# Optimization experiments

Measured on AMD Instinct MI355X. Metric: run time of the kernel, lower is better.

## Reference

```python
import jax, jax.numpy as jnp
import numpy as np

SEQ_LEN, BATCH, INPUT_SIZE, HIDDEN = 512, 64, 256, 512


def setup_inputs() -> dict:
    key = jax.random.key(0)
    ks = jax.random.split(key, 5)
    s_in = 1.0 / np.sqrt(INPUT_SIZE)
    s_h = 1.0 / np.sqrt(HIDDEN)
    x = jax.random.normal(ks[0], (SEQ_LEN, BATCH, INPUT_SIZE), dtype=jnp.float32)
    # gate order: f, i, o, c  (matches the torch module's lin_W*/lin_U*)
    Wx = jax.random.uniform(ks[1], (4, HIDDEN, INPUT_SIZE), jnp.float32, -s_in, s_in)
    bx = jax.random.uniform(ks[2], (4, HIDDEN), jnp.float32, -s_in, s_in)
    Wh = jax.random.uniform(ks[3], (4, HIDDEN, HIDDEN), jnp.float32, -s_h, s_h)
    bh = jax.random.uniform(ks[4], (4, HIDDEN), jnp.float32, -s_h, s_h)
    return {"x": x, "Wx": Wx, "bx": bx, "Wh": Wh, "bh": bh}


def reference(x, Wx, bx, Wh, bh):
    # x: [T, B, I]; Wx: [4, H, I]; Wh: [4, H, H]; biases: [4, H] (gate order f,i,o,c)
    T, B, _ = x.shape
    H = Wh.shape[-1]
    # Precompute input projections for all timesteps (batched GEMM): [T, 4, B, H]
    gx = jnp.einsum('tbi,ghi->tgbh', x, Wx) + bx[:, None, :]

    def step(carry, gx_t):
        h_prev, c_prev = carry
        gh = jnp.einsum('bh,gkh->gbk', h_prev, Wh) + bh[:, None, :]  # [4, B, H]
        g = gx_t + gh
        f = jax.nn.sigmoid(g[0])
        i = jax.nn.sigmoid(g[1])
        o = jax.nn.sigmoid(g[2])
        c = f * c_prev + i * jnp.tanh(g[3])
        h = o * jnp.tanh(c)
        return (h, c), h

    h0 = jnp.zeros((B, H), dtype=x.dtype)
    c0 = jnp.zeros((B, H), dtype=x.dtype)
    (h_last, c_last), h_seq = jax.lax.scan(step, (h0, c0), gx)
    return h_seq, h_last, c_last
```

## Files before the change

kernel.cpp:

```cpp
#include <hip/hip_runtime.h>
#include <hip/hip_cooperative_groups.h>
#include <math.h>

namespace cg = cooperative_groups;

#define TT 512
#define BB 64
#define II 256
#define HH 512

#define NTHREADS 512
#define NGRP 4
#define NCT  16
#define NBLOCKS (NGRP*NCT)

#define KPAD 776

typedef _Float16 f16x8 __attribute__((ext_vector_type(8)));
typedef _Float16 f16x4 __attribute__((ext_vector_type(4)));
typedef float    f32x4 __attribute__((ext_vector_type(4)));

__device__ __forceinline__ float sig_(float v)  { return 1.0f / (1.0f + __expf(-v)); }
__device__ __forceinline__ float tanh_(float v) { float e = __expf(2.0f * v); return 1.0f - 2.0f / (e + 1.0f); }

__global__ void __launch_bounds__(NTHREADS, 2)
lstm_mfma2(const float* __restrict__ x,
           const float* __restrict__ Wx,
           const float* __restrict__ bx,
           const float* __restrict__ Wh,
           const float* __restrict__ bh,
           float* __restrict__ out,
           unsigned int* __restrict__ flags,
           unsigned int* __restrict__ hbuf)
{
    __shared__ _Float16 AL[16 * KPAD];
    __shared__ float    exch[8 * 16 * 20];

    cg::grid_group grid = cg::this_grid();

    const int blk  = blockIdx.x;
    const int grp  = blk & 3;
    const int b0   = grp * 16;
    const int ct   = blk >> 2;
    const int hblk = ct * 32;

    const int tid = threadIdx.x;
    const int wv  = tid >> 6;
    const int L   = tid & 63;
    const int n   = L & 15;
    const int qd  = L >> 4;

    const int g  = n & 3;
    const int hu = hblk + wv * 4 + (n >> 2);
    f16x8 bfr[24];
    #pragma unroll
    for (int kc = 0; kc < 24; ++kc) {
        int k0 = kc * 32 + qd * 8;
        const float* src = (kc < 8)
            ? (Wx + ((size_t)g * HH + hu) * II + k0)
            : (Wh + ((size_t)g * HH + hu) * HH + (k0 - 256));
        float4 u0 = ((const float4*)src)[0];
        float4 u1 = ((const float4*)src)[1];
        f16x8 b = { (_Float16)u0.x, (_Float16)u0.y, (_Float16)u0.z, (_Float16)u0.w,
                    (_Float16)u1.x, (_Float16)u1.y, (_Float16)u1.z, (_Float16)u1.w };
        bfr[kc] = b;
    }

    const int be  = L >> 2;
    const int hle = L & 3;
    const int he  = hblk + wv * 4 + hle;
    float bias4[4];
    #pragma unroll
    for (int g2 = 0; g2 < 4; ++g2) bias4[g2] = bx[g2 * HH + he] + bh[g2 * HH + he];

    if (tid == 0)
        __hip_atomic_store(&flags[grp * 64 + ct], 0u,
                           __ATOMIC_RELAXED, __HIP_MEMORY_SCOPE_AGENT);
    grid.sync();

    const size_t HSEQ = (size_t)TT * BB * HH;
    float c_state = 0.0f;
    float* exchW = &exch[wv * 16 * 20];

    for (int t = 0; t < TT; ++t) {
        #pragma unroll
        for (int i = 0; i < 2; ++i) {
            int ch = tid + i * NTHREADS;
            int row = ch >> 6, pos = ch & 63;
            float4 v = ((const float4*)(x + ((size_t)t * BB + b0 + row) * II))[pos];
            f16x4 p = { (_Float16)v.x, (_Float16)v.y, (_Float16)v.z, (_Float16)v.w };
            *(f16x4*)&AL[row * KPAD + pos * 4] = p;
        }

        if (t > 0 && wv == 0) {
            const unsigned int* fp = flags + grp * 64;
            for (;;) {
                unsigned f = (L < NCT)
                    ? __hip_atomic_load(&fp[L], __ATOMIC_RELAXED, __HIP_MEMORY_SCOPE_AGENT)
                    : 0xFFFFFFFFu;
                if (__all((int)(f >= (unsigned)t))) break;
                __builtin_amdgcn_s_sleep(1);
            }
        }
        __syncthreads();

        if (t > 0) {
            const unsigned long long* hsrc =
                (const unsigned long long*)(hbuf + (size_t)(t & 1) * (BB * 256));
            #pragma unroll
            for (int i = 0; i < 4; ++i) {
                int ch = tid + i * NTHREADS;
                int row = ch >> 7, pos = ch & 127;
                unsigned long long u = __hip_atomic_load(
                    hsrc + (size_t)(b0 + row) * 128 + pos,
                    __ATOMIC_RELAXED, __HIP_MEMORY_SCOPE_AGENT);
                *(unsigned long long*)((char*)AL + row * (KPAD * 2) + II * 2 + pos * 8) = u;
            }
            __syncthreads();
        }

        const char* Ab = (const char*)AL + n * (KPAD * 2) + qd * 16;
        f32x4 acc = { 0.f, 0.f, 0.f, 0.f };
        #pragma unroll
        for (int kc = 0; kc < 8; ++kc) {
            f16x8 a = *(const f16x8*)(Ab + kc * 64);
            acc = __builtin_amdgcn_mfma_f32_16x16x32_f16(a, bfr[kc], acc, 0, 0, 0);
        }
        if (t > 0) {
            #pragma unroll
            for (int kc = 8; kc < 24; ++kc) {
                f16x8 a = *(const f16x8*)(Ab + kc * 64);
                acc = __builtin_amdgcn_mfma_f32_16x16x32_f16(a, bfr[kc], acc, 0, 0, 0);
            }
        }

        #pragma unroll
        for (int r = 0; r < 4; ++r)
            exchW[(qd * 4 + r) * 20 + n] = acc[r];
        float4 pre4 = *(const float4*)&exchW[be * 20 + hle * 4];

        float pf = pre4.x + bias4[0];
        float pi = pre4.y + bias4[1];
        float po = pre4.z + bias4[2];
        float pc = pre4.w + bias4[3];
        float fg = sig_(pf), ig = sig_(pi), og = sig_(po);
        float cn = fg * c_state + ig * tanh_(pc);
        float hv = og * tanh_(cn);
        c_state = cn;

        out[((size_t)t * BB + b0 + be) * HH + he] = hv;
        if (t == TT - 1) {
            size_t r = (size_t)(b0 + be) * HH + he;
            out[HSEQ + r] = hv;
            out[HSEQ + (size_t)BB * HH + r] = cn;
        }

        {
            union { _Float16 f; unsigned short u; } cv; cv.f = (_Float16)hv;
            unsigned mine  = cv.u;
            unsigned other = (unsigned)__shfl_xor((int)mine, 1, 64);
            if ((hle & 1) == 0) {
                unsigned pk = mine | (other << 16);
                unsigned int* hdst = hbuf + (size_t)((t + 1) & 1) * (BB * 256);
                __hip_atomic_store(&hdst[(unsigned)(b0 + be) * 256 + (unsigned)(he >> 1)],
                                   pk, __ATOMIC_RELAXED, __HIP_MEMORY_SCOPE_AGENT);
            }
        }

        __syncthreads();
        if (t != TT - 1 && tid == 0)
            __hip_atomic_store(&flags[grp * 64 + ct], (unsigned)(t + 1),
                               __ATOMIC_RELAXED, __HIP_MEMORY_SCOPE_AGENT);
    }
}

extern "C" void kernel_launch(void* const* d_in, const int* in_sizes, int n_in,
                              void* d_out, int out_size, void* d_ws, size_t ws_size,
                              hipStream_t stream)
{
    const float* x  = (const float*)d_in[0];
    const float* Wx = (const float*)d_in[1];
    const float* bx = (const float*)d_in[2];
    const float* Wh = (const float*)d_in[3];
    const float* bh = (const float*)d_in[4];
    float* out = (float*)d_out;

    unsigned int* flags = (unsigned int*)d_ws;
    unsigned int* hbuf  = (unsigned int*)((char*)d_ws + 4096);

    void* args[] = { (void*)&x, (void*)&Wx, (void*)&bx, (void*)&Wh, (void*)&bh,
                     (void*)&out, (void*)&flags, (void*)&hbuf };
    hipLaunchCooperativeKernel((const void*)lstm_mfma2,
                               dim3(NBLOCKS), dim3(NTHREADS),
                               args, 0, stream);
}
```

Baseline: 1.674 ms.

## Shorten LSTM step critical path: precompute x-projection before flag wait, load h directly into registers

Computes the input-projection MFMAs before spinning on the cross-block flags, so the x part overlaps with waiting on other blocks. The h operand is loaded straight from global memory into MFMA registers instead of being staged through LDS, which removes a barrier and an LDS round trip. Four independent accumulators break the MFMA dependency chain. Output stores move after the flag publish, and syncthreads is replaced by lighter custom barriers. The risks are more register pressure from holding the h fragments and subtle memory-ordering issues from the hand-written barriers.

Result: slower. 4.675 ms (+179.3%).

```diff
diff --git a/kernel.cpp b/kernel.cpp
--- a/kernel.cpp
+++ b/kernel.cpp
@@ -14,7 +14,7 @@
 #define NCT  16
 #define NBLOCKS (NGRP*NCT)
 
-#define KPAD 776
+#define XPAD 264
 
 typedef _Float16 f16x8 __attribute__((ext_vector_type(8)));
 typedef _Float16 f16x4 __attribute__((ext_vector_type(4)));
@@ -23,8 +23,22 @@
 __device__ __forceinline__ float sig_(float v)  { return 1.0f / (1.0f + __expf(-v)); }
 __device__ __forceinline__ float tanh_(float v) { float e = __expf(2.0f * v); return 1.0f - 2.0f / (e + 1.0f); }
 
-__global__ void __launch_bounds__(NTHREADS, 2)
-lstm_mfma2(const float* __restrict__ x,
+__device__ __forceinline__ void barrier_lds() {
+    __builtin_amdgcn_sched_barrier(0);
+    asm volatile("s_waitcnt lgkmcnt(0)" ::: "memory");
+    __builtin_amdgcn_s_barrier();
+    __builtin_amdgcn_sched_barrier(0);
+}
+__device__ __forceinline__ void barrier_raw() {
+    __builtin_amdgcn_sched_barrier(0);
+    asm volatile("" ::: "memory");
+    __builtin_amdgcn_s_barrier();
+    asm volatile("" ::: "memory");
+    __builtin_amdgcn_sched_barrier(0);
+}
+
+__global__ void __launch_bounds__(NTHREADS, 1)
+lstm_short(const float* __restrict__ x,
            const float* __restrict__ Wx,
            const float* __restrict__ bx,
            const float* __restrict__ Wh,
@@ -33,8 +47,8 @@
            unsigned int* __restrict__ flags,
            unsigned int* __restrict__ hbuf)
 {
-    __shared__ _Float16 AL[16 * KPAD];
-    __shared__ float    exch[8 * 16 * 20];
+    __shared__ __align__(16) _Float16 AL[16 * XPAD];
+    __shared__ __align__(16) float    exch[8 * 16 * 20];
 
     cg::grid_group grid = cg::this_grid();
 
@@ -82,6 +96,9 @@
     float c_state = 0.0f;
     float* exchW = &exch[wv * 16 * 20];
 
+    const unsigned long long* hrow0 =
+        (const unsigned long long*)hbuf + (size_t)(b0 + n) * 128 + qd * 2;
+
     for (int t = 0; t < TT; ++t) {
         #pragma unroll
         for (int i = 0; i < 2; ++i) {
@@ -89,7 +106,19 @@
             int row = ch >> 6, pos = ch & 63;
             float4 v = ((const float4*)(x + ((size_t)t * BB + b0 + row) * II))[pos];
             f16x4 p = { (_Float16)v.x, (_Float16)v.y, (_Float16)v.z, (_Float16)v.w };
-            *(f16x4*)&AL[row * KPAD + pos * 4] = p;
+            *(f16x4*)&AL[row * XPAD + pos * 4] = p;
+        }
+        barrier_lds();
+
+        const char* Ax = (const char*)AL + n * (XPAD * 2) + qd * 16;
+        f32x4 c0 = {0,0,0,0}, c1 = {0,0,0,0}, c2 = {0,0,0,0}, c3 = {0,0,0,0};
+        #pragma unroll
+        for (int kc = 0; kc < 8; ++kc) {
+            f16x8 a = *(const f16x8*)(Ax + kc * 64);
+            if      ((kc & 3) == 0) c0 = __builtin_amdgcn_mfma_f32_16x16x32_f16(a, bfr[kc], c0, 0, 0, 0);
+            else if ((kc & 3) == 1) c1 = __builtin_amdgcn_mfma_f32_16x16x32_f16(a, bfr[kc], c1, 0, 0, 0);
+            else if ((kc & 3) == 2) c2 = __builtin_amdgcn_mfma_f32_16x16x32_f16(a, bfr[kc], c2, 0, 0, 0);
+            else                    c3 = __builtin_amdgcn_mfma_f32_16x16x32_f16(a, bfr[kc], c3, 0, 0, 0);
         }
 
         if (t > 0 && wv == 0) {
@@ -102,37 +131,30 @@
                 __builtin_amdgcn_s_sleep(1);
             }
         }
-        __syncthreads();
+        barrier_raw();
 
         if (t > 0) {
-            const unsigned long long* hsrc =
-                (const unsigned long long*)(hbuf + (size_t)(t & 1) * (BB * 256));
+            const unsigned long long* hb = hrow0 + (size_t)(t & 1) * (BB * 128);
+            unsigned long long hq[16][2];
             #pragma unroll
-            for (int i = 0; i < 4; ++i) {
-                int ch = tid + i * NTHREADS;
-                int row = ch >> 7, pos = ch & 127;
-                unsigned long long u = __hip_atomic_load(
-                    hsrc + (size_t)(b0 + row) * 128 + pos,
-                    __ATOMIC_RELAXED, __HIP_MEMORY_SCOPE_AGENT);
-                *(unsigned long long*)((char*)AL + row * (KPAD * 2) + II * 2 + pos * 8) = u;
-            }
-            __syncthreads();
-        }
-
-        const char* Ab = (const char*)AL + n * (KPAD * 2) + qd * 16;
-        f32x4 acc = { 0.f, 0.f, 0.f, 0.f };
-        #pragma unroll
-        for (int kc = 0; kc < 8; ++kc) {
-            f16x8 a = *(const f16x8*)(Ab + kc * 64);
-            acc = __builtin_amdgcn_mfma_f32_16x16x32_f16(a, bfr[kc], acc, 0, 0, 0);
-        }
-        if (t > 0) {
+            for (int kc = 0; kc < 16; ++kc) {
+                hq[kc][0] = __hip_atomic_load(hb + kc * 8 + 0,
+                                              __ATOMIC_RELAXED, __HIP_MEMORY_SCOPE_AGENT);
+                hq[kc][1] = __hip_atomic_load(hb + kc * 8 + 1,
+                                              __ATOMIC_RELAXED, __HIP_MEMORY_SCOPE_AGENT);
+            }
             #pragma unroll
-            for (int kc = 8; kc < 24; ++kc) {
-                f16x8 a = *(const f16x8*)(Ab + kc * 64);
-                acc = __builtin_amdgcn_mfma_f32_16x16x32_f16(a, bfr[kc], acc, 0, 0, 0);
-            }
-        }
+            for (int kc = 0; kc < 16; ++kc) {
+                union { unsigned long long q[2]; f16x8 v; } cvt;
+                cvt.q[0] = hq[kc][0]; cvt.q[1] = hq[kc][1];
+                f16x8 a = cvt.v;
+                if      ((kc & 3) == 0) c0 = __builtin_amdgcn_mfma_f32_16x16x32_f16(a, bfr[kc + 8], c0, 0, 0, 0);
+                else if ((kc & 3) == 1) c1 = __builtin_amdgcn_mfma_f32_16x16x32_f16(a, bfr[kc + 8], c1, 0, 0, 0);
+                else if ((kc & 3) == 2) c2 = __builtin_amdgcn_mfma_f32_16x16x32_f16(a, bfr[kc + 8], c2, 0, 0, 0);
+                else                    c3 = __builtin_amdgcn_mfma_f32_16x16x32_f16(a, bfr[kc + 8], c3, 0, 0, 0);
+            }
+        }
+        f32x4 acc = (c0 + c1) + (c2 + c3);
 
         #pragma unroll
         for (int r = 0; r < 4; ++r)
@@ -147,13 +169,6 @@
         float cn = fg * c_state + ig * tanh_(pc);
         float hv = og * tanh_(cn);
         c_state = cn;
-
-        out[((size_t)t * BB + b0 + be) * HH + he] = hv;
-        if (t == TT - 1) {
-            size_t r = (size_t)(b0 + be) * HH + he;
-            out[HSEQ + r] = hv;
-            out[HSEQ + (size_t)BB * HH + r] = cn;
-        }
 
         {
             union { _Float16 f; unsigned short u; } cv; cv.f = (_Float16)hv;
@@ -167,10 +182,20 @@
             }
         }
 
-        __syncthreads();
+        __builtin_amdgcn_sched_barrier(0);
+        asm volatile("s_waitcnt vmcnt(0) lgkmcnt(0)" ::: "memory");
+        __builtin_amdgcn_s_barrier();
+        __builtin_amdgcn_sched_barrier(0);
         if (t != TT - 1 && tid == 0)
             __hip_atomic_store(&flags[grp * 64 + ct], (unsigned)(t + 1),
                                __ATOMIC_RELAXED, __HIP_MEMORY_SCOPE_AGENT);
+
+        out[((size_t)t * BB + b0 + be) * HH + he] = hv;
+        if (t == TT - 1) {
+            size_t r = (size_t)(b0 + be) * HH + he;
+            out[HSEQ + r] = hv;
+            out[HSEQ + (size_t)BB * HH + r] = cn;
+        }
     }
 }
 
@@ -190,7 +215,7 @@
 
     void* args[] = { (void*)&x, (void*)&Wx, (void*)&bx, (void*)&Wh, (void*)&bh,
                      (void*)&out, (void*)&flags, (void*)&hbuf };
-    hipLaunchCooperativeKernel((const void*)lstm_mfma2,
+    hipLaunchCooperativeKernel((const void*)lstm_short,
                                dim3(NBLOCKS), dim3(NTHREADS),
                                args, 0, stream);
 }
```
